# Kernel tuning notes

Hardware: AMD Instinct MI355X
Metric: run time of the kernel (lower is better)

Reference implementation:

```python
import jax, jax.numpy as jnp
import numpy as np

N_AGENTS = 8
N_ACTIONS = 16
SAMPLE = 16
STATE_DIM = 256
EMBED = 256
IN_DIM = N_AGENTS * N_ACTIONS + STATE_DIM  # 384


def setup_inputs() -> dict:
    key = jax.random.key(0)
    ks = jax.random.split(key, 12)
    bs, t = 32, 32
    s = 0.05
    return {
        "states": jax.random.normal(ks[0], (bs, t, STATE_DIM), jnp.float32),
        "agent_qs": jax.random.normal(ks[1], (bs, t, N_AGENTS, N_ACTIONS), jnp.float32),
        "W1": jax.random.normal(ks[2], (IN_DIM, EMBED), jnp.float32) * s,
        "b1": jnp.zeros((EMBED,), jnp.float32),
        "W2": jax.random.normal(ks[3], (EMBED, EMBED), jnp.float32) * s,
        "b2": jnp.zeros((EMBED,), jnp.float32),
        "W3": jax.random.normal(ks[4], (EMBED, 1), jnp.float32) * s,
        "b3": jnp.zeros((1,), jnp.float32),
        "Vw1": jax.random.normal(ks[5], (STATE_DIM, EMBED), jnp.float32) * s,
        "Vb1": jnp.zeros((EMBED,), jnp.float32),
        "Vw2": jax.random.normal(ks[6], (EMBED, 1), jnp.float32) * s,
        "Vb2": jnp.zeros((1,), jnp.float32),
    }


def reference(states, agent_qs, W1, b1, W2, b2, W3, b3, Vw1, Vb1, Vw2, Vb2):
    bs, t = states.shape[0], states.shape[1]
    B = bs * t
    A, NA, S, sd = N_AGENTS, N_ACTIONS, SAMPLE, STATE_DIM
    st = states.reshape(B, sd)
    qs = agent_qs.reshape(B, A, NA)

    # --- sample grand coalitions (random permutation per (B,S) row) ---
    perm_key = jax.random.key(42)
    u = jax.random.uniform(perm_key, (B, S, A))
    pos = jnp.argsort(u, axis=-1)          # grand_coalitions_pos: agent i -> position pos[i]
    inv = jnp.argsort(pos, axis=-1)        # grand_coalitions: position j -> agent inv[j]

    indiv = jax.nn.one_hot(pos, A, dtype=st.dtype)                         # (B,S,A,A)
    subcoal = (jnp.arange(A)[None, None, None, :] <= pos[..., None]).astype(st.dtype)
    no_i = subcoal - indiv                                                 # coalition members excl. self

    # reorder agent qs along position dim: reordered[b,s,j,:] = qs[b, inv[b,s,j], :]
    reordered = jnp.take_along_axis(
        jnp.broadcast_to(qs[:, None], (B, S, A, NA)), inv[..., None], axis=2)

    # (B,S,A,A,NA): detach contribution of other coalition members
    coal = (jax.lax.stop_gradient(reordered[:, :, None] * no_i[..., None])
            + reordered[:, :, None] * indiv[..., None])

    x = coal.reshape(B * S * A, A * NA)
    stx = jnp.broadcast_to(st[:, None, None], (B, S, A, sd)).reshape(B * S * A, sd)
    inp = jnp.concatenate([stx, x], axis=1)

    h = jax.nn.relu(inp @ W1 + b1)
    h = jax.nn.relu(h @ W2 + b2)
    advs = h @ W3 + b3
    v = jax.nn.relu(stx @ Vw1 + Vb1) @ Vw2 + Vb2

    marginal = (advs + v).reshape(B, S, A)
    shapley = marginal.mean(axis=1)        # mean over samples
    return shapley.reshape(bs, t, A)
```

## Files before the change

kernel.cpp:

```cpp
#include <hip/hip_runtime.h>


#define A_N   8
#define NA_N  16
#define S_N   16
#define SD    256
#define EMB   256
#define B_TOT 1024

typedef __bf16 bf16x8 __attribute__((ext_vector_type(8)));
typedef float  f32x4  __attribute__((ext_vector_type(4)));

__device__ __forceinline__ f32x4 splat4(float v) {
  f32x4 x; x[0] = v; x[1] = v; x[2] = v; x[3] = v; return x;
}
__device__ __forceinline__ bf16x8 zero8() {
  bf16x8 z;
#pragma unroll
  for (int j = 0; j < 8; ++j) z[j] = (__bf16)0.0f;
  return z;
}

__device__ __forceinline__ float jax_uniform(unsigned idx) {
  const unsigned ks0 = 0u, ks1 = 42u, ks2 = 0x1BD11BDAu ^ 42u;
  unsigned x0 = 0u + ks0;
  unsigned x1 = idx + ks1;
#define TF_RND(r) { x0 += x1; x1 = (x1 << (r)) | (x1 >> (32 - (r))); x1 ^= x0; }
  TF_RND(13) TF_RND(15) TF_RND(26) TF_RND(6)  x0 += ks1; x1 += ks2 + 1u;
  TF_RND(17) TF_RND(29) TF_RND(16) TF_RND(24) x0 += ks2; x1 += ks0 + 2u;
  TF_RND(13) TF_RND(15) TF_RND(26) TF_RND(6)  x0 += ks0; x1 += ks1 + 3u;
  TF_RND(17) TF_RND(29) TF_RND(16) TF_RND(24) x0 += ks1; x1 += ks2 + 4u;
  TF_RND(13) TF_RND(15) TF_RND(26) TF_RND(6)  x0 += ks2; x1 += ks0 + 5u;
#undef TF_RND
  const unsigned bits = x0 ^ x1;
  return __uint_as_float((bits >> 9) | 0x3F800000u) - 1.0f;
}

__global__ __launch_bounds__(256) void pack_kernel(
    const float* __restrict__ W1, const float* __restrict__ W2,
    const float* __restrict__ Vw1, __bf16* __restrict__ W1b_bf,
    __bf16* __restrict__ W2_bf, __bf16* __restrict__ PW_bf) {
  const int ts = blockIdx.x * 256 + threadIdx.x;
  if (ts < 4096) {
    const int t = ts >> 10, rem = ts & 1023, u = rem >> 6, L = rem & 63;
    const int q = L >> 4, l15 = L & 15;
#pragma unroll
    for (int j = 0; j < 8; ++j) {
      const int k = t * 32 + q * 8 + j, nn = u * 16 + l15;
      W1b_bf[ts * 8 + j] = (__bf16)W1[(SD + k) * EMB + nn];
    }
  } else if (ts < 12288) {
    const int ts2 = ts - 4096;
    const int t = ts2 >> 10, rem = ts2 & 1023, u = rem >> 6, L = rem & 63;
    const int q = L >> 4, l15 = L & 15;
#pragma unroll
    for (int j = 0; j < 8; ++j) {
      const int k = t * 32 + q * 8 + j, nn = u * 16 + l15;
      W2_bf[ts2 * 8 + j] = (__bf16)W2[k * EMB + nn];
    }
  } else {
    const int ts3 = ts - 12288;
    const int t = ts3 >> 11, rem = ts3 & 2047, u = rem >> 6, L = rem & 63;
    const int q = L >> 4, l15 = L & 15;
#pragma unroll
    for (int j = 0; j < 8; ++j) {
      const int k = t * 32 + q * 8 + j, nn = u * 16 + l15;
      const float v = (nn < EMB) ? W1[k * EMB + nn]
                                 : Vw1[k * EMB + (nn - EMB)];
      PW_bf[ts3 * 8 + j] = (__bf16)v;
    }
  }
}

__global__ __launch_bounds__(256) void prep_mfma_kernel(
    const float* __restrict__ states, const float* __restrict__ b1,
    const float* __restrict__ Vb1, const float* __restrict__ Vw2,
    const __bf16* __restrict__ PW_bf, float* __restrict__ sW,
    float* __restrict__ vv) {
  const int mi = blockIdx.x >> 2;
  const int ni = blockIdx.x & 3;
  const int n = threadIdx.x;
  const int w = n >> 6, L = n & 63, q = L >> 4, l15 = L & 15;

  f32x4 acc[4][2];
#pragma unroll
  for (int ui = 0; ui < 2; ++ui) {
    const int col = (ni * 8 + w * 2 + ui) * 16 + l15;
    const float bias = (col < EMB) ? b1[col] : Vb1[col - EMB];
#pragma unroll
    for (int mt = 0; mt < 4; ++mt) acc[mt][ui] = splat4(bias);
  }

#pragma unroll 2
  for (int t = 0; t < 8; ++t) {
    bf16x8 bfr[2];
#pragma unroll
    for (int ui = 0; ui < 2; ++ui) {
      const int u = ni * 8 + w * 2 + ui;
      bfr[ui] = *(const bf16x8*)&PW_bf[((t * 32 + u) * 64 + L) * 8];
    }
#pragma unroll
    for (int mt = 0; mt < 4; ++mt) {
      const float* srow = &states[(mi * 64 + mt * 16 + l15) * SD + t * 32 + q * 8];
      bf16x8 af;
#pragma unroll
      for (int j = 0; j < 8; ++j) af[j] = (__bf16)srow[j];
#pragma unroll
      for (int ui = 0; ui < 2; ++ui)
        acc[mt][ui] = __builtin_amdgcn_mfma_f32_16x16x32_bf16(
            af, bfr[ui], acc[mt][ui], 0, 0, 0);
    }
  }

  if (ni < 2) {
#pragma unroll
    for (int ui = 0; ui < 2; ++ui) {
      const int col = (ni * 8 + w * 2 + ui) * 16 + l15;
#pragma unroll
      for (int mt = 0; mt < 4; ++mt)
#pragma unroll
        for (int r = 0; r < 4; ++r)
          sW[(mi * 64 + mt * 16 + q * 4 + r) * EMB + col] = acc[mt][ui][r];
    }
  } else {
#pragma unroll
    for (int mt = 0; mt < 4; ++mt) {
#pragma unroll
      for (int r = 0; r < 4; ++r) {
        float p = 0.f;
#pragma unroll
        for (int ui = 0; ui < 2; ++ui) {
          const int colV = (ni * 8 + w * 2 + ui) * 16 + l15 - EMB;
          p = fmaf(fmaxf(acc[mt][ui][r], 0.f), Vw2[colV], p);
        }
#pragma unroll
        for (int off = 1; off < 16; off <<= 1) p += __shfl_xor(p, off);
        if (l15 == 0)
          atomicAdd(&vv[mi * 64 + mt * 16 + q * 4 + r], p);
      }
    }
  }
}

__global__ __launch_bounds__(256, 4) void main_kernel(
    const float* __restrict__ agent_qs, const float* __restrict__ b2g,
    const float* __restrict__ W3, const float* __restrict__ b3,
    const float* __restrict__ Vb2, const float* __restrict__ sW,
    const float* __restrict__ vv, const __bf16* __restrict__ W1b_bf,
    const __bf16* __restrict__ W2_bf, float* __restrict__ out) {
  __shared__ bf16x8 h1_l[32 * 64];
  __shared__ __attribute__((aligned(16))) __bf16 qs_bf[A_N * NA_N];
  __shared__ float u_l[128];
  __shared__ int   inv_l[128];
  __shared__ int   pos_l[128];
  __shared__ float adv_part[4][64];
  __shared__ float marg_l[128];

  const int b = blockIdx.x;
  const int n = threadIdx.x;
  const int w = n >> 6, L = n & 63, q = L >> 4, l15 = L & 15;

  if (n < 128) {
    qs_bf[n] = (__bf16)agent_qs[b * 128 + n];
    u_l[n] = jax_uniform((unsigned)(b * 128 + n));
  }
  __syncthreads();

  if (n < 128) {
    const int s = n >> 3, a = n & 7;
    const float u = u_l[n];
    int r = 0;
#pragma unroll
    for (int a2 = 0; a2 < A_N; ++a2) {
      const float u2 = u_l[s * 8 + a2];
      r += (u2 < u || (u2 == u && a2 < a)) ? 1 : 0;
    }
    inv_l[n] = r;
    pos_l[s * 8 + r] = a;
  }
  __syncthreads();

  const int i_pref  = l15 & 7;
  const int sl_half = l15 >> 3;
  const int jq      = q >> 1;
  const int na0     = (q & 1) * 8;

  for (int p = 0; p < 2; ++p) {
#pragma unroll 1
    for (int nh = 0; nh < 2; ++nh) {
      f32x4 acc[4][2];
#pragma unroll
      for (int i = 0; i < 2; ++i) {
        const float sv = sW[b * EMB + (w * 4 + nh * 2 + i) * 16 + l15];
#pragma unroll
        for (int mt = 0; mt < 4; ++mt) acc[mt][i] = splat4(sv);
      }
#pragma unroll 2
      for (int t = 0; t < 4; ++t) {
        const int jcoal = t * 2 + jq;
        const bool on = (jcoal <= i_pref);
        bf16x8 bfr[2];
#pragma unroll
        for (int i = 0; i < 2; ++i)
          bfr[i] = *(const bf16x8*)
              &W1b_bf[((t * 16 + w * 4 + nh * 2 + i) * 64 + L) * 8];
#pragma unroll
        for (int mt = 0; mt < 4; ++mt) {
          const int ag = inv_l[(p * 8 + mt * 2 + sl_half) * 8 + jcoal];
          const bf16x8 qv = *(const bf16x8*)&qs_bf[ag * NA_N + na0];
          const bf16x8 af = on ? qv : zero8();
#pragma unroll
          for (int i = 0; i < 2; ++i)
            acc[mt][i] = __builtin_amdgcn_mfma_f32_16x16x32_bf16(
                af, bfr[i], acc[mt][i], 0, 0, 0);
        }
      }
      __bf16* h1e = (__bf16*)h1_l;
#pragma unroll
      for (int i = 0; i < 2; ++i) {
        const int c = (w * 4 + nh * 2 + i) * 16 + l15;
        const int t2 = c >> 5, q2 = (c >> 3) & 3, j2 = l15 & 7;
#pragma unroll
        for (int mt = 0; mt < 4; ++mt) {
#pragma unroll
          for (int r = 0; r < 4; ++r) {
            const float v = fmaxf(acc[mt][i][r], 0.f);
            h1e[(((t2 * 4 + mt) * 64) + q2 * 16 + q * 4 + r) * 8 + j2] =
                (__bf16)v;
          }
        }
      }
    }
    __syncthreads();

    float psum[4][4];
#pragma unroll
    for (int mt = 0; mt < 4; ++mt)
#pragma unroll
      for (int r = 0; r < 4; ++r) psum[mt][r] = 0.f;

#pragma unroll 1
    for (int nh = 0; nh < 2; ++nh) {
      f32x4 acc[4][2];
#pragma unroll
      for (int i = 0; i < 2; ++i) {
        const float bv = b2g[(w * 4 + nh * 2 + i) * 16 + l15];
#pragma unroll
        for (int mt = 0; mt < 4; ++mt) acc[mt][i] = splat4(bv);
      }
#pragma unroll 2
      for (int t = 0; t < 8; ++t) {
        bf16x8 bfr[2];
#pragma unroll
        for (int i = 0; i < 2; ++i)
          bfr[i] = *(const bf16x8*)
              &W2_bf[((t * 16 + w * 4 + nh * 2 + i) * 64 + L) * 8];
#pragma unroll
        for (int mt = 0; mt < 4; ++mt) {
          const bf16x8 af = h1_l[(t * 4 + mt) * 64 + L];
#pragma unroll
          for (int i = 0; i < 2; ++i)
            acc[mt][i] = __builtin_amdgcn_mfma_f32_16x16x32_bf16(
                af, bfr[i], acc[mt][i], 0, 0, 0);
        }
      }
#pragma unroll
      for (int i = 0; i < 2; ++i) {
        const float w3v = W3[(w * 4 + nh * 2 + i) * 16 + l15];
#pragma unroll
        for (int mt = 0; mt < 4; ++mt)
#pragma unroll
          for (int r = 0; r < 4; ++r)
            psum[mt][r] = fmaf(fmaxf(acc[mt][i][r], 0.f), w3v, psum[mt][r]);
      }
    }

#pragma unroll
    for (int mt = 0; mt < 4; ++mt) {
#pragma unroll
      for (int r = 0; r < 4; ++r) {
        float sum = psum[mt][r];
#pragma unroll
        for (int off = 1; off < 16; off <<= 1) sum += __shfl_xor(sum, off);
        if (l15 == 0) adv_part[w][mt * 16 + q * 4 + r] = sum;
      }
    }
    __syncthreads();
    if (n < 64)
      marg_l[p * 64 + n] = adv_part[0][n] + adv_part[1][n] +
                           adv_part[2][n] + adv_part[3][n];
    __syncthreads();
  }

  if (n < A_N) {
    float sh = 0.f;
#pragma unroll
    for (int s = 0; s < S_N; ++s) sh += marg_l[s * 8 + pos_l[s * 8 + n]];
    out[b * A_N + n] = sh * (1.f / 16.f) + b3[0] + Vb2[0] + vv[b];
  }
}

extern "C" void kernel_launch(void* const* d_in, const int* in_sizes, int n_in,
                              void* d_out, int out_size, void* d_ws,
                              size_t ws_size, hipStream_t stream) {
  const float* states   = (const float*)d_in[0];
  const float* agent_qs = (const float*)d_in[1];
  const float* W1       = (const float*)d_in[2];
  const float* b1       = (const float*)d_in[3];
  const float* W2       = (const float*)d_in[4];
  const float* b2       = (const float*)d_in[5];
  const float* W3       = (const float*)d_in[6];
  const float* b3       = (const float*)d_in[7];
  const float* Vw1      = (const float*)d_in[8];
  const float* Vb1      = (const float*)d_in[9];
  const float* Vw2      = (const float*)d_in[10];
  const float* Vb2      = (const float*)d_in[11];
  float* out = (float*)d_out;

  char* ws = (char*)d_ws;
  float*  sW     = (float*)(ws);
  float*  vv     = (float*)(ws + 1048576);
  __bf16* W1b_bf = (__bf16*)(ws + 1052672);
  __bf16* W2_bf  = (__bf16*)(ws + 1118208);
  __bf16* PW_bf  = (__bf16*)(ws + 1249280);

  hipMemsetAsync(vv, 0, B_TOT * sizeof(float), stream);
  pack_kernel<<<112, 256, 0, stream>>>(W1, W2, Vw1, W1b_bf, W2_bf, PW_bf);
  prep_mfma_kernel<<<64, 256, 0, stream>>>(states, b1, Vb1, Vw2, PW_bf,
                                           sW, vv);
  main_kernel<<<B_TOT, 256, 0, stream>>>(agent_qs, b2, W3, b3, Vb2, sW, vv,
                                         W1b_bf, W2_bf, out);
}
```

Baseline: 124.9 us.

## Merge pack and prep kernels, drop memset and atomics for value-head partials

Folds the weight-pack and state-projection kernels into one launch: the first 48 blocks pack W1b/W2 to bf16 while the remaining blocks compute the states projection, reading W1/Vw1 fp32 directly instead of through a packed PW buffer. The value-head reduction now writes two per-half partial arrays through shared memory instead of atomically adding into a memset buffer, which removes the memset launch. In the main kernel, per-column sW/b2/W3 values are hoisted into registers, and the final cross-wave reduction is moved to the output step, removing one barrier per pass. The cost is strided fp32 weight loads in the prep blocks.

```diff
diff --git a/kernel.cpp b/kernel.cpp
--- a/kernel.cpp
+++ b/kernel.cpp
@@ -36,50 +36,42 @@
   return __uint_as_float((bits >> 9) | 0x3F800000u) - 1.0f;
 }
 
-__global__ __launch_bounds__(256) void pack_kernel(
-    const float* __restrict__ W1, const float* __restrict__ W2,
-    const float* __restrict__ Vw1, __bf16* __restrict__ W1b_bf,
-    __bf16* __restrict__ W2_bf, __bf16* __restrict__ PW_bf) {
-  const int ts = blockIdx.x * 256 + threadIdx.x;
-  if (ts < 4096) {
-    const int t = ts >> 10, rem = ts & 1023, u = rem >> 6, L = rem & 63;
-    const int q = L >> 4, l15 = L & 15;
-#pragma unroll
-    for (int j = 0; j < 8; ++j) {
-      const int k = t * 32 + q * 8 + j, nn = u * 16 + l15;
-      W1b_bf[ts * 8 + j] = (__bf16)W1[(SD + k) * EMB + nn];
-    }
-  } else if (ts < 12288) {
-    const int ts2 = ts - 4096;
-    const int t = ts2 >> 10, rem = ts2 & 1023, u = rem >> 6, L = rem & 63;
-    const int q = L >> 4, l15 = L & 15;
-#pragma unroll
-    for (int j = 0; j < 8; ++j) {
-      const int k = t * 32 + q * 8 + j, nn = u * 16 + l15;
-      W2_bf[ts2 * 8 + j] = (__bf16)W2[k * EMB + nn];
-    }
-  } else {
-    const int ts3 = ts - 12288;
-    const int t = ts3 >> 11, rem = ts3 & 2047, u = rem >> 6, L = rem & 63;
-    const int q = L >> 4, l15 = L & 15;
-#pragma unroll
-    for (int j = 0; j < 8; ++j) {
-      const int k = t * 32 + q * 8 + j, nn = u * 16 + l15;
-      const float v = (nn < EMB) ? W1[k * EMB + nn]
-                                 : Vw1[k * EMB + (nn - EMB)];
-      PW_bf[ts3 * 8 + j] = (__bf16)v;
-    }
-  }
-}
-
-__global__ __launch_bounds__(256) void prep_mfma_kernel(
-    const float* __restrict__ states, const float* __restrict__ b1,
-    const float* __restrict__ Vb1, const float* __restrict__ Vw2,
-    const __bf16* __restrict__ PW_bf, float* __restrict__ sW,
-    float* __restrict__ vv) {
-  const int mi = blockIdx.x >> 2;
-  const int ni = blockIdx.x & 3;
+__global__ __launch_bounds__(256) void prep_pack_kernel(
+    const float* __restrict__ states, const float* __restrict__ W1,
+    const float* __restrict__ b1, const float* __restrict__ W2,
+    const float* __restrict__ Vw1, const float* __restrict__ Vb1,
+    const float* __restrict__ Vw2, float* __restrict__ sW,
+    float* __restrict__ vpart, __bf16* __restrict__ W1b_bf,
+    __bf16* __restrict__ W2_bf) {
   const int n = threadIdx.x;
+
+  if (blockIdx.x < 48) {
+    const int ts = blockIdx.x * 256 + n;
+    if (ts < 4096) {
+      const int t = ts >> 10, rem = ts & 1023, u = rem >> 6, L = rem & 63;
+      const int q = L >> 4, l15 = L & 15;
+#pragma unroll
+      for (int j = 0; j < 8; ++j) {
+        const int k = t * 32 + q * 8 + j, nn = u * 16 + l15;
+        W1b_bf[ts * 8 + j] = (__bf16)W1[(SD + k) * EMB + nn];
+      }
+    } else {
+      const int ts2 = ts - 4096;
+      const int t = ts2 >> 10, rem = ts2 & 1023, u = rem >> 6, L = rem & 63;
+      const int q = L >> 4, l15 = L & 15;
+#pragma unroll
+      for (int j = 0; j < 8; ++j) {
+        const int k = t * 32 + q * 8 + j, nn = u * 16 + l15;
+        W2_bf[ts2 * 8 + j] = (__bf16)W2[k * EMB + nn];
+      }
+    }
+    return;
+  }
+
+  __shared__ float vred[4][64];
+  const int blk = blockIdx.x - 48;
+  const int mi = blk >> 2;
+  const int ni = blk & 3;
   const int w = n >> 6, L = n & 63, q = L >> 4, l15 = L & 15;
 
   f32x4 acc[4][2];
@@ -96,12 +88,19 @@
     bf16x8 bfr[2];
 #pragma unroll
     for (int ui = 0; ui < 2; ++ui) {
-      const int u = ni * 8 + w * 2 + ui;
-      bfr[ui] = *(const bf16x8*)&PW_bf[((t * 32 + u) * 64 + L) * 8];
+      const int nn = (ni * 8 + w * 2 + ui) * 16 + l15;
+#pragma unroll
+      for (int j = 0; j < 8; ++j) {
+        const int k = t * 32 + q * 8 + j;
+        const float v = (nn < EMB) ? W1[k * EMB + nn]
+                                   : Vw1[k * EMB + (nn - EMB)];
+        bfr[ui][j] = (__bf16)v;
+      }
     }
 #pragma unroll
     for (int mt = 0; mt < 4; ++mt) {
-      const float* srow = &states[(mi * 64 + mt * 16 + l15) * SD + t * 32 + q * 8];
+      const float* srow =
+          &states[(mi * 64 + mt * 16 + l15) * SD + t * 32 + q * 8];
       bf16x8 af;
 #pragma unroll
       for (int j = 0; j < 8; ++j) af[j] = (__bf16)srow[j];
@@ -135,10 +134,13 @@
         }
 #pragma unroll
         for (int off = 1; off < 16; off <<= 1) p += __shfl_xor(p, off);
-        if (l15 == 0)
-          atomicAdd(&vv[mi * 64 + mt * 16 + q * 4 + r], p);
-      }
-    }
+        if (l15 == 0) vred[w][mt * 16 + q * 4 + r] = p;
+      }
+    }
+    __syncthreads();
+    if (n < 64)
+      vpart[(ni - 2) * B_TOT + mi * 64 + n] =
+          vred[0][n] + vred[1][n] + vred[2][n] + vred[3][n];
   }
 }
 
@@ -146,15 +148,14 @@
     const float* __restrict__ agent_qs, const float* __restrict__ b2g,
     const float* __restrict__ W3, const float* __restrict__ b3,
     const float* __restrict__ Vb2, const float* __restrict__ sW,
-    const float* __restrict__ vv, const __bf16* __restrict__ W1b_bf,
+    const float* __restrict__ vpart, const __bf16* __restrict__ W1b_bf,
     const __bf16* __restrict__ W2_bf, float* __restrict__ out) {
   __shared__ bf16x8 h1_l[32 * 64];
   __shared__ __attribute__((aligned(16))) __bf16 qs_bf[A_N * NA_N];
   __shared__ float u_l[128];
   __shared__ int   inv_l[128];
   __shared__ int   pos_l[128];
-  __shared__ float adv_part[4][64];
-  __shared__ float marg_l[128];
+  __shared__ float adv_part[4][128];
 
   const int b = blockIdx.x;
   const int n = threadIdx.x;
@@ -163,6 +164,14 @@
   if (n < 128) {
     qs_bf[n] = (__bf16)agent_qs[b * 128 + n];
     u_l[n] = jax_uniform((unsigned)(b * 128 + n));
+  }
+  float sWv[4], b2v[4], w3v[4];
+#pragma unroll
+  for (int j = 0; j < 4; ++j) {
+    const int c = (w * 4 + j) * 16 + l15;
+    sWv[j] = sW[b * EMB + c];
+    b2v[j] = b2g[c];
+    w3v[j] = W3[c];
   }
   __syncthreads();
 
@@ -191,9 +200,8 @@
       f32x4 acc[4][2];
 #pragma unroll
       for (int i = 0; i < 2; ++i) {
-        const float sv = sW[b * EMB + (w * 4 + nh * 2 + i) * 16 + l15];
-#pragma unroll
-        for (int mt = 0; mt < 4; ++mt) acc[mt][i] = splat4(sv);
+#pragma unroll
+        for (int mt = 0; mt < 4; ++mt) acc[mt][i] = splat4(sWv[nh * 2 + i]);
       }
 #pragma unroll 2
       for (int t = 0; t < 4; ++t) {
@@ -244,9 +252,8 @@
       f32x4 acc[4][2];
 #pragma unroll
       for (int i = 0; i < 2; ++i) {
-        const float bv = b2g[(w * 4 + nh * 2 + i) * 16 + l15];
-#pragma unroll
-        for (int mt = 0; mt < 4; ++mt) acc[mt][i] = splat4(bv);
+#pragma unroll
+        for (int mt = 0; mt < 4; ++mt) acc[mt][i] = splat4(b2v[nh * 2 + i]);
       }
 #pragma unroll 2
       for (int t = 0; t < 8; ++t) {
@@ -266,12 +273,12 @@
       }
 #pragma unroll
       for (int i = 0; i < 2; ++i) {
-        const float w3v = W3[(w * 4 + nh * 2 + i) * 16 + l15];
 #pragma unroll
         for (int mt = 0; mt < 4; ++mt)
 #pragma unroll
           for (int r = 0; r < 4; ++r)
-            psum[mt][r] = fmaf(fmaxf(acc[mt][i][r], 0.f), w3v, psum[mt][r]);
+            psum[mt][r] = fmaf(fmaxf(acc[mt][i][r], 0.f), w3v[nh * 2 + i],
+                               psum[mt][r]);
       }
     }
 
@@ -282,21 +289,22 @@
         float sum = psum[mt][r];
 #pragma unroll
         for (int off = 1; off < 16; off <<= 1) sum += __shfl_xor(sum, off);
-        if (l15 == 0) adv_part[w][mt * 16 + q * 4 + r] = sum;
-      }
-    }
-    __syncthreads();
-    if (n < 64)
-      marg_l[p * 64 + n] = adv_part[0][n] + adv_part[1][n] +
-                           adv_part[2][n] + adv_part[3][n];
+        if (l15 == 0) adv_part[w][p * 64 + mt * 16 + q * 4 + r] = sum;
+      }
+    }
     __syncthreads();
   }
 
   if (n < A_N) {
     float sh = 0.f;
 #pragma unroll
-    for (int s = 0; s < S_N; ++s) sh += marg_l[s * 8 + pos_l[s * 8 + n]];
-    out[b * A_N + n] = sh * (1.f / 16.f) + b3[0] + Vb2[0] + vv[b];
+    for (int s = 0; s < S_N; ++s) {
+      const int idx = (s >> 3) * 64 + (s & 7) * 8 + pos_l[s * 8 + n];
+      sh += adv_part[0][idx] + adv_part[1][idx] +
+            adv_part[2][idx] + adv_part[3][idx];
+    }
+    out[b * A_N + n] = sh * (1.f / 16.f) + b3[0] + Vb2[0] +
+                       vpart[b] + vpart[B_TOT + b];
   }
 }
 
@@ -319,15 +327,12 @@
 
   char* ws = (char*)d_ws;
   float*  sW     = (float*)(ws);
-  float*  vv     = (float*)(ws + 1048576);
-  __bf16* W1b_bf = (__bf16*)(ws + 1052672);
-  __bf16* W2_bf  = (__bf16*)(ws + 1118208);
-  __bf16* PW_bf  = (__bf16*)(ws + 1249280);
-
-  hipMemsetAsync(vv, 0, B_TOT * sizeof(float), stream);
-  pack_kernel<<<112, 256, 0, stream>>>(W1, W2, Vw1, W1b_bf, W2_bf, PW_bf);
-  prep_mfma_kernel<<<64, 256, 0, stream>>>(states, b1, Vb1, Vw2, PW_bf,
-                                           sW, vv);
-  main_kernel<<<B_TOT, 256, 0, stream>>>(agent_qs, b2, W3, b3, Vb2, sW, vv,
-                                         W1b_bf, W2_bf, out);
-}
+  float*  vpart  = (float*)(ws + 1048576);
+  __bf16* W1b_bf = (__bf16*)(ws + 1057792);
+  __bf16* W2_bf  = (__bf16*)(ws + 1123328);
+
+  prep_pack_kernel<<<112, 256, 0, stream>>>(states, W1, b1, W2, Vw1, Vb1,
+                                            Vw2, sW, vpart, W1b_bf, W2_bf);
+  main_kernel<<<B_TOT, 256, 0, stream>>>(agent_qs, b2, W3, b3, Vb2, sW,
+                                         vpart, W1b_bf, W2_bf, out);
+}
```

Measured after the change: 123.9 us. About the same (-0.8%).
